# Kernel tuning notes

Measured on AMD Instinct MI355X. Metric: run time of the kernel, lower is better.

The kernel has to match this reference:

```python
import jax, jax.numpy as jnp
import numpy as np

N = 50000      # nodes
E = 800000     # edges (before self-loops)
H = 2          # attention heads
C = 64         # hidden_channels (per-head out since concat=False)
L = 3          # num_layers - 2 conv blocks
OUT = 128      # readout out_channels
G = 512        # num graphs
VOCAB = 100    # embedding table size
NEG_SLOPE = 0.2


def setup_inputs() -> dict:
    key = jax.random.key(0)
    ks = jax.random.split(key, 12)
    s = 1.0 / np.sqrt(C)
    x = jax.random.randint(ks[0], (N,), 0, VOCAB, dtype=jnp.int32)
    edge_index = jax.random.randint(ks[1], (2, E), 0, N, dtype=jnp.int32)
    batch = jnp.sort(jax.random.randint(ks[2], (N,), 0, G, dtype=jnp.int32))
    embed = jax.random.normal(ks[3], (VOCAB, C), dtype=jnp.float32) * s
    lin_W = jax.random.normal(ks[4], (L, C, C), dtype=jnp.float32) * s
    lin_b = jnp.zeros((L, C), dtype=jnp.float32)
    gat_Wl = jax.random.normal(ks[5], (L, C, H * C), dtype=jnp.float32) * s
    gat_bl = jnp.zeros((L, H * C), dtype=jnp.float32)
    gat_Wr = jax.random.normal(ks[6], (L, C, H * C), dtype=jnp.float32) * s
    gat_br = jnp.zeros((L, H * C), dtype=jnp.float32)
    gat_att = jax.random.normal(ks[7], (L, H, C), dtype=jnp.float32) * s
    gat_bias = jnp.zeros((L, C), dtype=jnp.float32)
    readout_W = jax.random.normal(ks[8], (C, OUT), dtype=jnp.float32) * s
    readout_b = jnp.zeros((OUT,), dtype=jnp.float32)
    return {"x": x, "edge_index": edge_index, "batch": batch, "num_graphs": G,
            "embed": embed, "lin_W": lin_W, "lin_b": lin_b,
            "gat_Wl": gat_Wl, "gat_bl": gat_bl, "gat_Wr": gat_Wr, "gat_br": gat_br,
            "gat_att": gat_att, "gat_bias": gat_bias,
            "readout_W": readout_W, "readout_b": readout_b}


def _gatv2_layer(h, src, dst, Wl, bl, Wr, br, att, bias):
    # lin_l -> source/message features, lin_r -> target features (PyG GATv2Conv)
    xl = (h @ Wl + bl).reshape(N, H, C)
    xr = (h @ Wr + br).reshape(N, H, C)
    # per-edge GATv2 score: a^T LeakyReLU(x_l[j] + x_r[i])
    e = jax.nn.leaky_relu(xl[src] + xr[dst], NEG_SLOPE)      # [E2,H,C]
    score = jnp.einsum('ehc,hc->eh', e, att)                 # [E2,H]
    # segment softmax over incoming edges of each dst node (stable)
    m = jax.lax.stop_gradient(jax.ops.segment_max(score, dst, num_segments=N))
    p = jnp.exp(score - m[dst])
    denom = jax.ops.segment_sum(p, dst, num_segments=N)      # [N,H]
    alpha = p / denom[dst]                                   # [E2,H]
    msg = xl[src] * alpha[:, :, None]                        # [E2,H,C]
    agg = jax.ops.segment_sum(msg, dst, num_segments=N)      # [N,H,C]
    return agg.mean(axis=1) + bias                           # concat=False -> head mean


def reference(x, edge_index, batch, num_graphs, embed, lin_W, lin_b,
              gat_Wl, gat_bl, gat_Wr, gat_br, gat_att, gat_bias,
              readout_W, readout_b):
    # add self loops (GATv2Conv default add_self_loops=True)
    loops = jnp.arange(N, dtype=edge_index.dtype)
    src = jnp.concatenate([edge_index[0], loops])
    dst = jnp.concatenate([edge_index[1], loops])
    h = embed[x]                                             # [N,C]
    for l in range(L):
        h = jax.nn.relu(h @ lin_W[l] + lin_b[l])             # dropout is a no-op in eval
        h = _gatv2_layer(h, src, dst, gat_Wl[l], gat_bl[l], gat_Wr[l], gat_br[l],
                         gat_att[l], gat_bias[l])
    out = h @ readout_W + readout_b                          # [N,OUT]
    return jax.ops.segment_sum(out, batch, num_segments=num_graphs)  # [G,OUT]
```

## Files before the change

kernel.cpp:

```cpp
#include <hip/hip_runtime.h>
#include <hip/hip_fp16.h>

#define N_NODES  50000
#define E_EDGES  800000
#define E_TOT    850000
#define H_HEADS  2
#define C_DIM    64
#define HC       128
#define L_LAYERS 3
#define OUT_DIM  128
#define G_GRAPHS 512
#define NEG_SLOPE 0.2f
#define NB       196
#define EPB      4096
#define BSTRIDE  4864

typedef float v2f __attribute__((ext_vector_type(2)));

__device__ __forceinline__ void lds_fence() { asm volatile("" ::: "memory"); }

__global__ void init_kernel(float* __restrict__ out, int* __restrict__ bwptr) {
    int i = blockIdx.x * 256 + threadIdx.x;
    if (i < G_GRAPHS * OUT_DIM) out[i] = 0.f;
    if (blockIdx.x == 0) bwptr[threadIdx.x] = 0;
}

__global__ void edge_partition_kernel(const int* __restrict__ srcs, const int* __restrict__ dsts,
                                      int* __restrict__ bwptr, unsigned int* __restrict__ ebuf) {
    __shared__ int hist[256];
    __shared__ int lscan[256];
    __shared__ int sExcl[256];
    __shared__ int lcnt[256];
    __shared__ int gbase[256];
    __shared__ unsigned int sval[EPB];
    __shared__ unsigned char sgid[EPB];
    int tid = threadIdx.x;
    int ebase = blockIdx.x * EPB;
    hist[tid] = 0;
    __syncthreads();
    unsigned int val[16];
    int gid[16];
#pragma unroll
    for (int i = 0; i < 16; i++) {
        int e = ebase + i * 256 + tid;
        if (e < E_TOT) {
            int s, d;
            if (e < E_EDGES) { s = srcs[e]; d = dsts[e]; }
            else             { s = d = e - E_EDGES; }
            val[i] = ((unsigned)s << 8) | (unsigned)(d & 255);
            gid[i] = d >> 8;
            atomicAdd(&hist[gid[i]], 1);
        } else gid[i] = -1;
    }
    __syncthreads();
    lscan[tid] = hist[tid];
    __syncthreads();
#pragma unroll
    for (int off = 1; off < 256; off <<= 1) {
        int t = (tid >= off) ? lscan[tid - off] : 0;
        __syncthreads();
        lscan[tid] += t;
        __syncthreads();
    }
    sExcl[tid] = lscan[tid] - hist[tid];
    lcnt[tid] = 0;
    __syncthreads();
#pragma unroll
    for (int i = 0; i < 16; i++) {
        if (gid[i] >= 0) {
            int off = atomicAdd(&lcnt[gid[i]], 1);
            int idx = sExcl[gid[i]] + off;
            sval[idx] = val[i];
            sgid[idx] = (unsigned char)gid[i];
        }
    }
    if (tid < NB) {
        int c = hist[tid];
        gbase[tid] = c ? atomicAdd(&bwptr[tid], c) : 0;
    }
    __syncthreads();
    int total = lscan[255];
    for (int idx = tid; idx < total; idx += 256) {
        int g = sgid[idx];
        ebuf[(size_t)g * BSTRIDE + gbase[g] + (idx - sExcl[g])] = sval[idx];
    }
}

__global__ void bucket_csr_kernel(const unsigned int* __restrict__ ebuf,
                                  const int* __restrict__ bwptr,
                                  int2* __restrict__ row_se,
                                  unsigned short* __restrict__ src_sorted) {
    __shared__ int hist[256];
    __shared__ int lcnt[256];
    __shared__ int wsum[4];
    int g = blockIdx.x, tid = threadIdx.x;
    int n0 = g << 8;
    int nodes = min(256, N_NODES - n0);
    int b0 = g * BSTRIDE;
    int cnt = bwptr[g];
    hist[tid] = 0;
    lcnt[tid] = 0;
    __syncthreads();
    for (int i = tid; i < cnt; i += 256) atomicAdd(&hist[ebuf[b0 + i] & 255], 1);
    __syncthreads();
    int c = hist[tid];
    int v = c;
    int lane = tid & 63, wid = tid >> 6;
#pragma unroll
    for (int off = 1; off < 64; off <<= 1) {
        int t = __shfl_up(v, off, 64);
        if (lane >= off) v += t;
    }
    if (lane == 63) wsum[wid] = v;
    __syncthreads();
    int woff = 0;
#pragma unroll
    for (int w = 0; w < 4; w++) if (w < wid) woff += wsum[w];
    v += woff;
    int nbase = b0 + v - c;
    if (tid < nodes) row_se[n0 + tid] = make_int2(nbase, nbase + c);
    __syncthreads();
    hist[tid] = nbase;
    __syncthreads();
    for (int i = tid; i < cnt; i += 256) {
        unsigned int e = ebuf[b0 + i];
        int dl = e & 255;
        int slot = hist[dl] + atomicAdd(&lcnt[dl], 1);
        src_sorted[slot] = (unsigned short)(e >> 8);
    }
}

__global__ void layer_lin_kernel(const float* __restrict__ h,
                                 const int* __restrict__ xs, const float* __restrict__ etab,
                                 int use_embed,
                                 const float* __restrict__ W, const float* __restrict__ b,
                                 const float* __restrict__ Wl, const float* __restrict__ bl,
                                 const float* __restrict__ Wr, const float* __restrict__ br,
                                 __half* __restrict__ xlh, __half* __restrict__ xrh) {
    __shared__ float sH[16 * 64];
    __shared__ float sH2[16 * 64];
    int tid = threadIdx.x;
    int base = blockIdx.x * 16;
#pragma unroll
    for (int i = 0; i < 4; i++) {
        int idx = tid + i * 256;
        int nn = base + (idx >> 6);
        int cc = idx & 63;
        float hv = 0.f;
        if (nn < N_NODES)
            hv = use_embed ? etab[xs[nn] * 64 + cc] : h[(size_t)nn * 64 + cc];
        sH[idx] = hv;
    }
    __syncthreads();
    {
        int c = tid & 63, g = tid >> 6;
        v2f a2[4];
#pragma unroll
        for (int n = 0; n < 4; n++) a2[n] = (v2f){b[c], 0.f};
        for (int k = 0; k < 64; k += 2) {
            v2f w2 = {W[k * 64 + c], W[(k + 1) * 64 + c]};
#pragma unroll
            for (int n = 0; n < 4; n++) {
                v2f hv2 = *(const v2f*)&sH[(g * 4 + n) * 64 + k];
                a2[n] = __builtin_elementwise_fma(hv2, w2, a2[n]);
            }
        }
#pragma unroll
        for (int n = 0; n < 4; n++)
            sH2[(g * 4 + n) * 64 + c] = fmaxf(a2[n].x + a2[n].y, 0.f);
    }
    __syncthreads();
    {
        int j = tid & 127, gg = tid >> 7;
        v2f accl2[8], accr2[8];
#pragma unroll
        for (int n = 0; n < 8; n++) {
            accl2[n] = (v2f){bl[j], 0.f};
            accr2[n] = (v2f){br[j], 0.f};
        }
        for (int k = 0; k < 64; k += 2) {
            v2f wl2 = {Wl[k * 128 + j], Wl[(k + 1) * 128 + j]};
            v2f wr2 = {Wr[k * 128 + j], Wr[(k + 1) * 128 + j]};
#pragma unroll
            for (int n = 0; n < 8; n++) {
                v2f hv2 = *(const v2f*)&sH2[(gg * 8 + n) * 64 + k];
                accl2[n] = __builtin_elementwise_fma(hv2, wl2, accl2[n]);
                accr2[n] = __builtin_elementwise_fma(hv2, wr2, accr2[n]);
            }
        }
        int hh = j >> 6, c = j & 63;
#pragma unroll
        for (int n = 0; n < 8; n++) {
            int node = base + gg * 8 + n;
            if (node < N_NODES) {
                size_t o = (size_t)node * 128 + c * 2 + hh;
                xlh[o] = __float2half(accl2[n].x + accl2[n].y);
                xrh[o] = __float2half(accr2[n].x + accr2[n].y);
            }
        }
    }
}

__global__ void __launch_bounds__(128)
gat_kernel(const __half2* __restrict__ xlh, const __half2* __restrict__ xrh2,
           const float* __restrict__ att, const int2* __restrict__ row_se,
           const unsigned short* __restrict__ src_sorted,
           const float* __restrict__ bias,
           float* __restrict__ h_out) {
    __shared__ __align__(16) float cbuf[2][8 * 132];
    int w = threadIdx.x >> 6;
    int d = blockIdx.x * 2 + w;
    if (d >= N_NODES) return;
    int lane = threadIdx.x & 63;
    int2 se = row_se[d];
    int r0 = se.x, r1 = se.y;
    float2 vrf = __half22float2(xrh2[(size_t)d * 64 + lane]);
    v2f vr2 = {vrf.x, vrf.y};
    v2f att2 = {att[lane], att[64 + lane]};
    float* cb = cbuf[w];
    int e_of = lane >> 3, p = lane & 7;

    float dpx = 0.f, dpy = 0.f;
    v2f ac0 = {0.f, 0.f}, ac1 = {0.f, 0.f};

#define GAT_LOAD(V, CB) do {                                                    \
        int lim_ = nchunk - 1;                                                  \
        _Pragma("unroll")                                                       \
        for (int e = 0; e < 8; e++) {                                           \
            int ee_ = (CB) + e;                                                 \
            int sv_ = __builtin_amdgcn_readlane(idx, (ee_ < nchunk) ? ee_ : lim_); \
            V[e] = xlh[(size_t)sv_ * 64 + lane];                                \
        }                                                                       \
    } while (0)

#define GAT_PROC(V, CB) do {                                                    \
        int rem_ = nchunk - (CB);                                               \
        v2f vf8[8];                                                             \
        _Pragma("unroll")                                                       \
        for (int e = 0; e < 8; e++) {                                           \
            float2 vf_ = __half22float2(V[e]);                                  \
            v2f vl2 = {vf_.x, vf_.y};                                           \
            vf8[e] = vl2;                                                       \
            v2f z = vl2 + vr2;                                                  \
            v2f t = __builtin_elementwise_max(z, z * NEG_SLOPE) * att2;         \
            *(v2f*)&cb[e * 132 + 2 * lane] = t;                                 \
        }                                                                       \
        lds_fence();                                                            \
        v2f s2 = {0.f, 0.f};                                                    \
        {                                                                       \
            const float4* row_ = (const float4*)&cb[e_of * 132 + p * 16];       \
            _Pragma("unroll")                                                   \
            for (int j = 0; j < 4; j++) {                                       \
                float4 f = row_[j];                                             \
                s2 += (v2f){f.x, f.y};                                          \
                s2 += (v2f){f.z, f.w};                                          \
            }                                                                   \
        }                                                                       \
        lds_fence();                                                            \
        _Pragma("unroll")                                                       \
        for (int off = 1; off <= 4; off <<= 1) {                                \
            v2f o_;                                                             \
            o_.x = __shfl_xor(s2.x, off, 64);                                   \
            o_.y = __shfl_xor(s2.y, off, 64);                                   \
            s2 += o_;                                                           \
        }                                                                       \
        float sx = s2.x, sy = s2.y;                                             \
        if (e_of >= rem_) { sx = -INFINITY; sy = -INFINITY; }                   \
        float wx = __expf(sx), wy = __expf(sy);                                 \
        dpx += wx; dpy += wy;                                                   \
        _Pragma("unroll")                                                       \
        for (int e = 0; e < 8; e++) {                                           \
            float swx = __int_as_float(__builtin_amdgcn_readlane(__float_as_int(wx), 8 * e)); \
            float swy = __int_as_float(__builtin_amdgcn_readlane(__float_as_int(wy), 8 * e)); \
            v2f w2 = {swx, swy};                                                \
            if (e & 1) ac1 = __builtin_elementwise_fma(w2, vf8[e], ac1);        \
            else       ac0 = __builtin_elementwise_fma(w2, vf8[e], ac0);        \
        }                                                                       \
    } while (0)

    for (int base = r0; base < r1; base += 64) {
        int a = base + lane;
        int idx = (int)src_sorted[(a < r1) ? a : (r1 - 1)];
        int nchunk = min(64, r1 - base);
        __half2 va[8], vb[8];
        GAT_LOAD(va, 0);
        int cb_i = 0;
        for (;;) {
            int nx = cb_i + 8;
            if (nx < nchunk) {
                GAT_LOAD(vb, nx);
                GAT_PROC(va, cb_i);
                cb_i = nx;
            } else {
                GAT_PROC(va, cb_i);
                break;
            }
            nx = cb_i + 8;
            if (nx < nchunk) {
                GAT_LOAD(va, nx);
                GAT_PROC(vb, cb_i);
                cb_i = nx;
            } else {
                GAT_PROC(vb, cb_i);
                break;
            }
        }
    }
#undef GAT_LOAD
#undef GAT_PROC

#pragma unroll
    for (int off = 8; off <= 32; off <<= 1) {
        dpx += __shfl_xor(dpx, off, 64);
        dpy += __shfl_xor(dpy, off, 64);
    }
    v2f acc = ac0 + ac1;
    h_out[(size_t)d * 64 + lane] = (acc.x / dpx + acc.y / dpy) * 0.5f + bias[lane];
}

__global__ void readout_kernel(const float* __restrict__ h, const float* __restrict__ W,
                               const float* __restrict__ b, const int* __restrict__ batch,
                               float* __restrict__ out) {
    __shared__ float sH[16 * 64];
    __shared__ int sB[16];
    int tid = threadIdx.x;
    int base = blockIdx.x * 16;
#pragma unroll
    for (int i = 0; i < 4; i++) {
        int idx = tid + i * 256;
        int nn = base + (idx >> 6);
        sH[idx] = (nn < N_NODES) ? h[(size_t)nn * 64 + (idx & 63)] : 0.f;
    }
    if (tid < 16) sB[tid] = (base + tid < N_NODES) ? batch[base + tid] : -1;
    __syncthreads();
    int j = tid & 127, gg = tid >> 7;
    float acc[8];
#pragma unroll
    for (int n = 0; n < 8; n++) acc[n] = b[j];
    for (int k = 0; k < 64; k++) {
        float wv = W[k * OUT_DIM + j];
#pragma unroll
        for (int n = 0; n < 8; n++) acc[n] = fmaf(sH[(gg * 8 + n) * 64 + k], wv, acc[n]);
    }
    float run = 0.f; int curb = -2;
#pragma unroll
    for (int n = 0; n < 8; n++) {
        int node = base + gg * 8 + n;
        int bb = (node < N_NODES) ? sB[gg * 8 + n] : -1;
        if (bb != curb) {
            if (curb >= 0) atomicAdd(&out[curb * OUT_DIM + j], run);
            run = 0.f; curb = bb;
        }
        if (bb >= 0) run += acc[n];
    }
    if (curb >= 0) atomicAdd(&out[curb * OUT_DIM + j], run);
}

extern "C" void kernel_launch(void* const* d_in, const int* in_sizes, int n_in,
                              void* d_out, int out_size, void* d_ws, size_t ws_size,
                              hipStream_t stream) {
    const int*   x        = (const int*)d_in[0];
    const int*   edge     = (const int*)d_in[1];
    const int*   batch    = (const int*)d_in[2];
    const float* embed    = (const float*)d_in[4];
    const float* lin_W    = (const float*)d_in[5];
    const float* lin_b    = (const float*)d_in[6];
    const float* gat_Wl   = (const float*)d_in[7];
    const float* gat_bl   = (const float*)d_in[8];
    const float* gat_Wr   = (const float*)d_in[9];
    const float* gat_br   = (const float*)d_in[10];
    const float* gat_att  = (const float*)d_in[11];
    const float* gat_bias = (const float*)d_in[12];
    const float* ro_W     = (const float*)d_in[13];
    const float* ro_b     = (const float*)d_in[14];
    float* out = (float*)d_out;

    const int* srcs = edge;
    const int* dsts = edge + E_EDGES;

    float* h    = (float*)d_ws;
    __half* xlh = (__half*)(h + (size_t)N_NODES * 64);
    __half* xrh = xlh + (size_t)N_NODES * HC;
    int2* row_se       = (int2*)(xrh + (size_t)N_NODES * HC);
    int* bwptr         = (int*)(row_se + N_NODES);
    unsigned int* ebuf = (unsigned int*)(bwptr + 256);
    unsigned short* src_sorted = (unsigned short*)(ebuf + (size_t)NB * BSTRIDE);

    const int T = 256;
    const int gInit = (G_GRAPHS * OUT_DIM + 255) / 256;
    const int gPart = (E_TOT + EPB - 1) / EPB;
    const int gLin  = (N_NODES + 15) / 16;
    const int gGat  = (N_NODES + 1) / 2;

    init_kernel<<<gInit, T, 0, stream>>>(out, bwptr);
    edge_partition_kernel<<<gPart, T, 0, stream>>>(srcs, dsts, bwptr, ebuf);
    bucket_csr_kernel<<<NB, T, 0, stream>>>(ebuf, bwptr, row_se, src_sorted);

    for (int l = 0; l < L_LAYERS; l++) {
        layer_lin_kernel<<<gLin, T, 0, stream>>>(
            h, x, embed, (l == 0) ? 1 : 0,
            lin_W + (size_t)l * 64 * 64, lin_b + (size_t)l * 64,
            gat_Wl + (size_t)l * 64 * 128, gat_bl + (size_t)l * 128,
            gat_Wr + (size_t)l * 64 * 128, gat_br + (size_t)l * 128,
            xlh, xrh);
        gat_kernel<<<gGat, 128, 0, stream>>>(
            (const __half2*)xlh, (const __half2*)xrh, gat_att + (size_t)l * HC,
            row_se, src_sorted, gat_bias + (size_t)l * 64, h);
    }

    readout_kernel<<<gLin, T, 0, stream>>>(h, ro_W, ro_b, batch, out);
}
```

Measured before the change: 394.5 us.

## Merge init, edge partition and first-layer linear into one prelude kernel

Folds output zeroing, edge bucketing and the layer-0 embedding+linear projection into one launch with block-index-based role dispatch, so the independent dense work overlaps the edge partition. Partitioning now writes per-chunk fixed-size regions with per-chunk counts instead of global atomic bucket pointers, and the CSR kernel reads those regions with vector loads. The packed edge format changes to 16-bit src/dst fields. This removes two launches and global atomics, but adds padded buffer space and assumes at most RMAX edges per chunk per bucket, which holds only for roughly uniform destination distributions.

```diff
diff --git a/kernel.cpp b/kernel.cpp
--- a/kernel.cpp
+++ b/kernel.cpp
@@ -13,81 +13,148 @@
 #define NEG_SLOPE 0.2f
 #define NB       196
 #define EPB      4096
+#define NCHUNK   208
+#define RMAX     80
 #define BSTRIDE  4864
 
 typedef float v2f __attribute__((ext_vector_type(2)));
 
 __device__ __forceinline__ void lds_fence() { asm volatile("" ::: "memory"); }
 
-__global__ void init_kernel(float* __restrict__ out, int* __restrict__ bwptr) {
-    int i = blockIdx.x * 256 + threadIdx.x;
-    if (i < G_GRAPHS * OUT_DIM) out[i] = 0.f;
-    if (blockIdx.x == 0) bwptr[threadIdx.x] = 0;
-}
-
-__global__ void edge_partition_kernel(const int* __restrict__ srcs, const int* __restrict__ dsts,
-                                      int* __restrict__ bwptr, unsigned int* __restrict__ ebuf) {
-    __shared__ int hist[256];
-    __shared__ int lscan[256];
-    __shared__ int sExcl[256];
-    __shared__ int lcnt[256];
-    __shared__ int gbase[256];
-    __shared__ unsigned int sval[EPB];
-    __shared__ unsigned char sgid[EPB];
+__global__ void __launch_bounds__(256)
+prelude_kernel(const int* __restrict__ srcs, const int* __restrict__ dsts,
+               float* __restrict__ out,
+               int* __restrict__ rcnt, unsigned int* __restrict__ ebuf,
+               const int* __restrict__ xs, const float* __restrict__ etab,
+               const float* __restrict__ W, const float* __restrict__ b,
+               const float* __restrict__ Wl, const float* __restrict__ bl,
+               const float* __restrict__ Wr, const float* __restrict__ br,
+               __half* __restrict__ xlh, __half* __restrict__ xrh) {
+    __shared__ __align__(16) char smem[20480];
     int tid = threadIdx.x;
-    int ebase = blockIdx.x * EPB;
-    hist[tid] = 0;
-    __syncthreads();
-    unsigned int val[16];
-    int gid[16];
-#pragma unroll
-    for (int i = 0; i < 16; i++) {
-        int e = ebase + i * 256 + tid;
-        if (e < E_TOT) {
-            int s, d;
-            if (e < E_EDGES) { s = srcs[e]; d = dsts[e]; }
-            else             { s = d = e - E_EDGES; }
-            val[i] = ((unsigned)s << 8) | (unsigned)(d & 255);
-            gid[i] = d >> 8;
-            atomicAdd(&hist[gid[i]], 1);
-        } else gid[i] = -1;
-    }
-    __syncthreads();
-    lscan[tid] = hist[tid];
-    __syncthreads();
-#pragma unroll
-    for (int off = 1; off < 256; off <<= 1) {
-        int t = (tid >= off) ? lscan[tid - off] : 0;
-        __syncthreads();
-        lscan[tid] += t;
-        __syncthreads();
-    }
-    sExcl[tid] = lscan[tid] - hist[tid];
-    lcnt[tid] = 0;
-    __syncthreads();
-#pragma unroll
-    for (int i = 0; i < 16; i++) {
-        if (gid[i] >= 0) {
-            int off = atomicAdd(&lcnt[gid[i]], 1);
-            int idx = sExcl[gid[i]] + off;
-            sval[idx] = val[i];
-            sgid[idx] = (unsigned char)gid[i];
-        }
-    }
-    if (tid < NB) {
-        int c = hist[tid];
-        gbase[tid] = c ? atomicAdd(&bwptr[tid], c) : 0;
-    }
-    __syncthreads();
-    int total = lscan[255];
-    for (int idx = tid; idx < total; idx += 256) {
-        int g = sgid[idx];
-        ebuf[(size_t)g * BSTRIDE + gbase[g] + (idx - sExcl[g])] = sval[idx];
+    int bid = blockIdx.x;
+
+    if (bid < NCHUNK) {
+        int* hist  = (int*)smem;
+        int* lscan = hist + 256;
+        int* sExcl = lscan + 256;
+        int* lcnt  = sExcl + 256;
+        unsigned int* sval = (unsigned int*)(lcnt + 256);
+
+        for (int i = bid * 256 + tid; i < G_GRAPHS * OUT_DIM; i += NCHUNK * 256)
+            out[i] = 0.f;
+
+        int ebase = bid * EPB;
+        hist[tid] = 0;
+        __syncthreads();
+        unsigned int val[16];
+        int gid[16];
+#pragma unroll
+        for (int i = 0; i < 16; i++) {
+            int e = ebase + i * 256 + tid;
+            if (e < E_TOT) {
+                int s, d;
+                if (e < E_EDGES) { s = srcs[e]; d = dsts[e]; }
+                else             { s = d = e - E_EDGES; }
+                val[i] = ((unsigned)s << 16) | (unsigned)d;
+                gid[i] = d >> 8;
+                atomicAdd(&hist[gid[i]], 1);
+            } else gid[i] = -1;
+        }
+        __syncthreads();
+        lscan[tid] = hist[tid];
+        __syncthreads();
+#pragma unroll
+        for (int off = 1; off < 256; off <<= 1) {
+            int t = (tid >= off) ? lscan[tid - off] : 0;
+            __syncthreads();
+            lscan[tid] += t;
+            __syncthreads();
+        }
+        sExcl[tid] = lscan[tid] - hist[tid];
+        lcnt[tid] = 0;
+        __syncthreads();
+#pragma unroll
+        for (int i = 0; i < 16; i++) {
+            if (gid[i] >= 0) {
+                int off = atomicAdd(&lcnt[gid[i]], 1);
+                sval[sExcl[gid[i]] + off] = val[i];
+            }
+        }
+        if (tid < NB) rcnt[bid * NB + tid] = hist[tid];
+        __syncthreads();
+        int total = lscan[255];
+        for (int idx = tid; idx < total; idx += 256) {
+            unsigned int v = sval[idx];
+            int g = (int)((v & 0xFFFFu) >> 8);
+            ebuf[((size_t)g * NCHUNK + bid) * RMAX + (idx - sExcl[g])] = v;
+        }
+    } else {
+        float* sH  = (float*)smem;
+        float* sH2 = sH + 16 * 64;
+        int base = (bid - NCHUNK) * 16;
+#pragma unroll
+        for (int i = 0; i < 4; i++) {
+            int idx = tid + i * 256;
+            int nn = base + (idx >> 6);
+            int cc = idx & 63;
+            float hv = 0.f;
+            if (nn < N_NODES) hv = etab[xs[nn] * 64 + cc];
+            sH[idx] = hv;
+        }
+        __syncthreads();
+        {
+            int c = tid & 63, g = tid >> 6;
+            v2f a2[4];
+#pragma unroll
+            for (int n = 0; n < 4; n++) a2[n] = (v2f){b[c], 0.f};
+            for (int k = 0; k < 64; k += 2) {
+                v2f w2 = {W[k * 64 + c], W[(k + 1) * 64 + c]};
+#pragma unroll
+                for (int n = 0; n < 4; n++) {
+                    v2f hv2 = *(const v2f*)&sH[(g * 4 + n) * 64 + k];
+                    a2[n] = __builtin_elementwise_fma(hv2, w2, a2[n]);
+                }
+            }
+#pragma unroll
+            for (int n = 0; n < 4; n++)
+                sH2[(g * 4 + n) * 64 + c] = fmaxf(a2[n].x + a2[n].y, 0.f);
+        }
+        __syncthreads();
+        {
+            int j = tid & 127, gg = tid >> 7;
+            v2f accl2[8], accr2[8];
+#pragma unroll
+            for (int n = 0; n < 8; n++) {
+                accl2[n] = (v2f){bl[j], 0.f};
+                accr2[n] = (v2f){br[j], 0.f};
+            }
+            for (int k = 0; k < 64; k += 2) {
+                v2f wl2 = {Wl[k * 128 + j], Wl[(k + 1) * 128 + j]};
+                v2f wr2 = {Wr[k * 128 + j], Wr[(k + 1) * 128 + j]};
+#pragma unroll
+                for (int n = 0; n < 8; n++) {
+                    v2f hv2 = *(const v2f*)&sH2[(gg * 8 + n) * 64 + k];
+                    accl2[n] = __builtin_elementwise_fma(hv2, wl2, accl2[n]);
+                    accr2[n] = __builtin_elementwise_fma(hv2, wr2, accr2[n]);
+                }
+            }
+            int hh = j >> 6, c = j & 63;
+#pragma unroll
+            for (int n = 0; n < 8; n++) {
+                int node = base + gg * 8 + n;
+                if (node < N_NODES) {
+                    size_t o = (size_t)node * 128 + c * 2 + hh;
+                    xlh[o] = __float2half(accl2[n].x + accl2[n].y);
+                    xrh[o] = __float2half(accr2[n].x + accr2[n].y);
+                }
+            }
+        }
     }
 }
 
 __global__ void bucket_csr_kernel(const unsigned int* __restrict__ ebuf,
-                                  const int* __restrict__ bwptr,
+                                  const int* __restrict__ rcnt,
                                   int2* __restrict__ row_se,
                                   unsigned short* __restrict__ src_sorted) {
     __shared__ int hist[256];
@@ -96,12 +163,20 @@
     int g = blockIdx.x, tid = threadIdx.x;
     int n0 = g << 8;
     int nodes = min(256, N_NODES - n0);
-    int b0 = g * BSTRIDE;
-    int cnt = bwptr[g];
     hist[tid] = 0;
     lcnt[tid] = 0;
     __syncthreads();
-    for (int i = tid; i < cnt; i += 256) atomicAdd(&hist[ebuf[b0 + i] & 255], 1);
+    for (int blk = tid; blk < NCHUNK; blk += 256) {
+        int c = rcnt[blk * NB + g];
+        const uint4* rp = (const uint4*)&ebuf[((size_t)g * NCHUNK + blk) * RMAX];
+        for (int i = 0; i < c; i += 4) {
+            uint4 v4 = rp[i >> 2];
+            if (i + 0 < c) atomicAdd(&hist[v4.x & 255], 1);
+            if (i + 1 < c) atomicAdd(&hist[v4.y & 255], 1);
+            if (i + 2 < c) atomicAdd(&hist[v4.z & 255], 1);
+            if (i + 3 < c) atomicAdd(&hist[v4.w & 255], 1);
+        }
+    }
     __syncthreads();
     int c = hist[tid];
     int v = c;
@@ -117,22 +192,26 @@
 #pragma unroll
     for (int w = 0; w < 4; w++) if (w < wid) woff += wsum[w];
     v += woff;
-    int nbase = b0 + v - c;
+    int nbase = g * BSTRIDE + v - c;
     if (tid < nodes) row_se[n0 + tid] = make_int2(nbase, nbase + c);
     __syncthreads();
     hist[tid] = nbase;
     __syncthreads();
-    for (int i = tid; i < cnt; i += 256) {
-        unsigned int e = ebuf[b0 + i];
-        int dl = e & 255;
-        int slot = hist[dl] + atomicAdd(&lcnt[dl], 1);
-        src_sorted[slot] = (unsigned short)(e >> 8);
+    for (int blk = tid; blk < NCHUNK; blk += 256) {
+        int c2 = rcnt[blk * NB + g];
+        const uint4* rp = (const uint4*)&ebuf[((size_t)g * NCHUNK + blk) * RMAX];
+        for (int i = 0; i < c2; i += 4) {
+            uint4 v4 = rp[i >> 2];
+            unsigned int vv0 = v4.x, vv1 = v4.y, vv2 = v4.z, vv3 = v4.w;
+            if (i + 0 < c2) { int dl = vv0 & 255; int slot = hist[dl] + atomicAdd(&lcnt[dl], 1); src_sorted[slot] = (unsigned short)(vv0 >> 16); }
+            if (i + 1 < c2) { int dl = vv1 & 255; int slot = hist[dl] + atomicAdd(&lcnt[dl], 1); src_sorted[slot] = (unsigned short)(vv1 >> 16); }
+            if (i + 2 < c2) { int dl = vv2 & 255; int slot = hist[dl] + atomicAdd(&lcnt[dl], 1); src_sorted[slot] = (unsigned short)(vv2 >> 16); }
+            if (i + 3 < c2) { int dl = vv3 & 255; int slot = hist[dl] + atomicAdd(&lcnt[dl], 1); src_sorted[slot] = (unsigned short)(vv3 >> 16); }
+        }
     }
 }
 
 __global__ void layer_lin_kernel(const float* __restrict__ h,
-                                 const int* __restrict__ xs, const float* __restrict__ etab,
-                                 int use_embed,
                                  const float* __restrict__ W, const float* __restrict__ b,
                                  const float* __restrict__ Wl, const float* __restrict__ bl,
                                  const float* __restrict__ Wr, const float* __restrict__ br,
@@ -146,10 +225,7 @@
         int idx = tid + i * 256;
         int nn = base + (idx >> 6);
         int cc = idx & 63;
-        float hv = 0.f;
-        if (nn < N_NODES)
-            hv = use_embed ? etab[xs[nn] * 64 + cc] : h[(size_t)nn * 64 + cc];
-        sH[idx] = hv;
+        sH[idx] = (nn < N_NODES) ? h[(size_t)nn * 64 + cc] : 0.f;
     }
     __syncthreads();
     {
@@ -382,23 +458,25 @@
     __half* xlh = (__half*)(h + (size_t)N_NODES * 64);
     __half* xrh = xlh + (size_t)N_NODES * HC;
     int2* row_se       = (int2*)(xrh + (size_t)N_NODES * HC);
-    int* bwptr         = (int*)(row_se + N_NODES);
-    unsigned int* ebuf = (unsigned int*)(bwptr + 256);
-    unsigned short* src_sorted = (unsigned short*)(ebuf + (size_t)NB * BSTRIDE);
+    int* rcnt          = (int*)(row_se + N_NODES);
+    unsigned int* ebuf = (unsigned int*)(rcnt + NCHUNK * NB);
+    unsigned short* src_sorted =
+        (unsigned short*)(ebuf + (size_t)NB * NCHUNK * RMAX + 4096);
 
     const int T = 256;
-    const int gInit = (G_GRAPHS * OUT_DIM + 255) / 256;
-    const int gPart = (E_TOT + EPB - 1) / EPB;
-    const int gLin  = (N_NODES + 15) / 16;
-    const int gGat  = (N_NODES + 1) / 2;
-
-    init_kernel<<<gInit, T, 0, stream>>>(out, bwptr);
-    edge_partition_kernel<<<gPart, T, 0, stream>>>(srcs, dsts, bwptr, ebuf);
-    bucket_csr_kernel<<<NB, T, 0, stream>>>(ebuf, bwptr, row_se, src_sorted);
-
-    for (int l = 0; l < L_LAYERS; l++) {
+    const int gLin = (N_NODES + 15) / 16;
+    const int gGat = (N_NODES + 1) / 2;
+
+    prelude_kernel<<<NCHUNK + gLin, T, 0, stream>>>(
+        srcs, dsts, out, rcnt, ebuf, x, embed,
+        lin_W, lin_b, gat_Wl, gat_bl, gat_Wr, gat_br, xlh, xrh);
+    bucket_csr_kernel<<<NB, T, 0, stream>>>(ebuf, rcnt, row_se, src_sorted);
+    gat_kernel<<<gGat, 128, 0, stream>>>(
+        (const __half2*)xlh, (const __half2*)xrh, gat_att,
+        row_se, src_sorted, gat_bias, h);
+    for (int l = 1; l < L_LAYERS; l++) {
         layer_lin_kernel<<<gLin, T, 0, stream>>>(
-            h, x, embed, (l == 0) ? 1 : 0,
+            h,
             lin_W + (size_t)l * 64 * 64, lin_b + (size_t)l * 64,
             gat_Wl + (size_t)l * 64 * 128, gat_bl + (size_t)l * 128,
             gat_Wr + (size_t)l * 64 * 128, gat_br + (size_t)l * 128,
@@ -407,6 +485,5 @@
             (const __half2*)xlh, (const __half2*)xrh, gat_att + (size_t)l * HC,
             row_se, src_sorted, gat_bias + (size_t)l * 64, h);
     }
-
     readout_kernel<<<gLin, T, 0, stream>>>(h, ro_W, ro_b, batch, out);
 }
```

Measured after the change: 619.1 us. +57.0%, slower.
